# Kernel optimization log

Measured on AMD Instinct MI355X. Metric: run time of the kernel, lower is better.

## Reference

```python
import jax, jax.numpy as jnp
import numpy as np

D_MODEL = 1024
D_FF = 4096


def _layernorm(x, gamma, beta, eps=1e-5):
    mu = jnp.mean(x, axis=-1, keepdims=True)
    var = jnp.var(x, axis=-1, keepdims=True)
    return (x - mu) * jax.lax.rsqrt(var + eps) * gamma + beta


def setup_inputs() -> dict:
    key = jax.random.key(0)
    ks = jax.random.split(key, 7)
    B, S = 4, 2048
    src = jax.random.normal(ks[0], (B, S, D_MODEL), dtype=jnp.float32)
    gamma1 = jnp.ones((D_MODEL,), jnp.float32)
    beta1 = jnp.zeros((D_MODEL,), jnp.float32)
    gamma2 = jnp.ones((D_MODEL,), jnp.float32)
    beta2 = jnp.zeros((D_MODEL,), jnp.float32)
    w1 = jax.random.normal(ks[1], (D_MODEL, D_FF), jnp.float32) * (1.0 / np.sqrt(D_MODEL))
    b1 = jnp.zeros((D_FF,), jnp.float32)
    w2 = jax.random.normal(ks[2], (D_FF, D_MODEL), jnp.float32) * (1.0 / np.sqrt(D_FF))
    b2 = jnp.zeros((D_MODEL,), jnp.float32)
    return {"src": src, "gamma1": gamma1, "beta1": beta1,
            "gamma2": gamma2, "beta2": beta2,
            "w1": w1, "b1": b1, "w2": w2, "b2": b2}


def reference(src, gamma1, beta1, gamma2, beta2, w1, b1, w2, b2):
    # Pre-LN self-attention (single head, Q=K=V=norm_x, no projections)
    norm_x = _layernorm(src, gamma1, beta1)
    dim_k = norm_x.shape[-1]
    scores = jnp.einsum('bqd,bkd->bqk', norm_x, norm_x) / jnp.sqrt(jnp.float32(dim_k))
    weights = jax.nn.softmax(scores, axis=-1)
    attn = jnp.einsum('bqk,bkd->bqd', weights, norm_x)
    x = src + attn  # dropout p=0 -> identity
    # Pre-LN FFN
    h = _layernorm(x, gamma2, beta2)
    h = jax.nn.gelu(h @ w1 + b1, approximate=False)
    h = h @ w2 + b2
    return h + x
```

## Files before the change

kernel.cpp:

```cpp
#include <hip/hip_runtime.h>
#include <hip/hip_bf16.h>
#include <math.h>

typedef __attribute__((ext_vector_type(8))) short s8vec;
typedef __attribute__((ext_vector_type(16))) float f32x16;
typedef __attribute__((ext_vector_type(4))) unsigned short us4;

__device__ __forceinline__ unsigned short f2bf(float f) {
  unsigned u = __float_as_uint(f);
  u = (u + 0x7fffu + ((u >> 16) & 1u)) >> 16;
  return (unsigned short)u;
}
__device__ __forceinline__ float bf2f(unsigned short u) {
  return __uint_as_float(((unsigned)u) << 16);
}

__device__ __forceinline__ float fast_gelu(float t) {
  float t2 = t * t;
  float u = t * (1.59576912f + 0.07135481f * t2);
  float e = __expf(-u);
  return t * __frcp_rn(1.0f + e);
}

__device__ __forceinline__ void async_ld16(const unsigned short* g, unsigned short* l) {
  __builtin_amdgcn_global_load_lds(
      (__attribute__((address_space(1))) void*)g,
      (__attribute__((address_space(3))) void*)l, 16, 0, 0);
}

template <int EPI>
__global__ __launch_bounds__(256) void gemm_nt(
    const unsigned short* __restrict__ A, const unsigned short* __restrict__ B,
    float* __restrict__ outF, unsigned short* __restrict__ outB,
    const float* __restrict__ bias, const float* __restrict__ res,
    int M, int N, int K,
    long long bA, long long bB, long long bO, long long bR, float scale)
{
  __shared__ __align__(16) unsigned short As[128 * 64];
  __shared__ __align__(16) unsigned short Bs[128 * 64];

  const int tid = threadIdx.x;
  const int w = tid >> 6;
  const int l = tid & 63;
  const int z = blockIdx.z;

  A += (size_t)z * bA;
  B += (size_t)z * bB;

  const size_t tileM = (size_t)blockIdx.y * 128;
  const size_t tileN = (size_t)blockIdx.x * 128;

  const int sRow = l >> 3;
  const int sChunk = (l & 7) ^ sRow;
  const unsigned short* aBase = A + (tileM + (w << 5) + sRow) * (size_t)K + (sChunk << 3);
  const unsigned short* bBase = B + (tileN + (w << 5) + sRow) * (size_t)K + (sChunk << 3);
  unsigned short* ldsA = &As[(w << 5) * 64];
  unsigned short* ldsB = &Bs[(w << 5) * 64];

  const int wm = (w >> 1) << 6;
  const int wn = (w & 1) << 6;
  const int fr = l & 31;
  const int fq = l >> 5;

  f32x16 acc[2][2] = {};

  for (int k0 = 0; k0 < K; k0 += 64) {
    __syncthreads();
#pragma unroll
    for (int i = 0; i < 4; ++i) {
      async_ld16(aBase + k0 + (size_t)(i << 3) * K, ldsA + (i << 3) * 64);
      async_ld16(bBase + k0 + (size_t)(i << 3) * K, ldsB + (i << 3) * 64);
    }
    __syncthreads();

#pragma unroll
    for (int s = 0; s < 4; ++s) {
      const int p = ((s << 1) + fq) ^ (fr & 7);
      s8vec af[2], bf[2];
#pragma unroll
      for (int i = 0; i < 2; ++i)
        af[i] = *(const s8vec*)&As[(wm + (i << 5) + fr) * 64 + (p << 3)];
#pragma unroll
      for (int j = 0; j < 2; ++j)
        bf[j] = *(const s8vec*)&Bs[(wn + (j << 5) + fr) * 64 + (p << 3)];
#pragma unroll
      for (int i = 0; i < 2; ++i)
#pragma unroll
        for (int j = 0; j < 2; ++j)
          acc[i][j] = __builtin_amdgcn_mfma_f32_32x32x16_bf16(af[i], bf[j], acc[i][j], 0, 0, 0);
    }
  }

  float* oF = outF + (size_t)z * bO;
  unsigned short* oB = outB + (size_t)z * bO;
  const float* rs = res + (size_t)z * bR;

  float bcol[2];
  if (EPI >= 2) {
#pragma unroll
    for (int j = 0; j < 2; ++j) bcol[j] = bias[tileN + wn + (j << 5) + fr];
  }

#pragma unroll
  for (int i = 0; i < 2; ++i) {
#pragma unroll
    for (int r = 0; r < 16; ++r) {
      const size_t row = tileM + wm + (i << 5) + (r & 3) + ((r >> 2) << 3) + (fq << 2);
      const size_t rb = row * (size_t)N;
#pragma unroll
      for (int j = 0; j < 2; ++j) {
        const size_t col = tileN + wn + (j << 5) + fr;
        const float v = acc[i][j][r];
        if (EPI == 0) {
          oB[rb + col] = f2bf(v * scale);
        } else if (EPI == 1) {
          oF[rb + col] = v + rs[rb + col];
        } else if (EPI == 2) {
          oB[rb + col] = f2bf(fast_gelu(v + bcol[j]));
        } else {
          oF[rb + col] = v + bcol[j] + rs[rb + col];
        }
      }
    }
  }
}

__global__ __launch_bounds__(256) void ln_row(
    const float* __restrict__ x, const float* __restrict__ gamma,
    const float* __restrict__ beta, unsigned short* __restrict__ out)
{
  const int row = blockIdx.x;
  const float4* xr = (const float4*)(x + (size_t)row * 1024);
  const int tid = threadIdx.x;
  float4 v = xr[tid];
  float s = v.x + v.y + v.z + v.w;
  float q = v.x * v.x + v.y * v.y + v.z * v.z + v.w * v.w;
#pragma unroll
  for (int off = 32; off > 0; off >>= 1) {
    s += __shfl_down(s, off);
    q += __shfl_down(q, off);
  }
  __shared__ float rs_[4], rq_[4];
  const int w = tid >> 6, l = tid & 63;
  if (l == 0) { rs_[w] = s; rq_[w] = q; }
  __syncthreads();
  s = rs_[0] + rs_[1] + rs_[2] + rs_[3];
  q = rq_[0] + rq_[1] + rq_[2] + rq_[3];
  const float mu = s * (1.0f / 1024.0f);
  const float var = q * (1.0f / 1024.0f) - mu * mu;
  const float rstd = rsqrtf(var + 1e-5f);
  const float4 g = ((const float4*)gamma)[tid];
  const float4 b = ((const float4*)beta)[tid];
  us4 o;
  o.x = f2bf((v.x - mu) * rstd * g.x + b.x);
  o.y = f2bf((v.y - mu) * rstd * g.y + b.y);
  o.z = f2bf((v.z - mu) * rstd * g.z + b.z);
  o.w = f2bf((v.w - mu) * rstd * g.w + b.w);
  ((us4*)(out + (size_t)row * 1024))[tid] = o;
}

__global__ __launch_bounds__(256) void softmax_row(
    const unsigned short* __restrict__ sc, unsigned short* __restrict__ pr)
{
  const int row = blockIdx.x;
  const s8vec* s8 = (const s8vec*)(sc + (size_t)row * 2048);
  const int tid = threadIdx.x;
  s8vec a = s8[tid];
  float x[8];
#pragma unroll
  for (int i = 0; i < 8; ++i) x[i] = bf2f((unsigned short)a[i]);
  float mx = x[0];
#pragma unroll
  for (int i = 1; i < 8; ++i) mx = fmaxf(mx, x[i]);
#pragma unroll
  for (int off = 32; off > 0; off >>= 1) mx = fmaxf(mx, __shfl_down(mx, off));
  __shared__ float red[4];
  const int w = tid >> 6, l = tid & 63;
  if (l == 0) red[w] = mx;
  __syncthreads();
  mx = fmaxf(fmaxf(red[0], red[1]), fmaxf(red[2], red[3]));
  __syncthreads();
  float e[8], s = 0.f;
#pragma unroll
  for (int i = 0; i < 8; ++i) { e[i] = __expf(x[i] - mx); s += e[i]; }
#pragma unroll
  for (int off = 32; off > 0; off >>= 1) s += __shfl_down(s, off);
  if (l == 0) red[w] = s;
  __syncthreads();
  s = red[0] + red[1] + red[2] + red[3];
  const float inv = 1.0f / s;
  s8vec o;
#pragma unroll
  for (int i = 0; i < 8; ++i) o[i] = (short)f2bf(e[i] * inv);
  ((s8vec*)(pr + (size_t)row * 2048))[tid] = o;
}

template <bool BF16IN>
__global__ __launch_bounds__(256) void transpose_conv(
    const void* __restrict__ in_, unsigned short* __restrict__ out,
    int R, int C, long long bIn, long long bOut)
{
  __shared__ float tile[32][33];
  const int z = blockIdx.z;
  const int tx = threadIdx.x, ty = threadIdx.y;
  const int c0 = blockIdx.x * 32, r0 = blockIdx.y * 32;
  if (BF16IN) {
    const unsigned short* in = (const unsigned short*)in_ + (size_t)z * bIn;
    for (int i = ty; i < 32; i += 8)
      tile[i][tx] = bf2f(in[(size_t)(r0 + i) * C + c0 + tx]);
  } else {
    const float* in = (const float*)in_ + (size_t)z * bIn;
    for (int i = ty; i < 32; i += 8)
      tile[i][tx] = in[(size_t)(r0 + i) * C + c0 + tx];
  }
  __syncthreads();
  unsigned short* o = out + (size_t)z * bOut;
  for (int i = ty; i < 32; i += 8)
    o[(size_t)(c0 + i) * R + r0 + tx] = f2bf(tile[tx][i]);
}

extern "C" void kernel_launch(void* const* d_in, const int* in_sizes, int n_in,
                              void* d_out, int out_size, void* d_ws, size_t ws_size,
                              hipStream_t stream)
{
  (void)in_sizes; (void)n_in; (void)out_size; (void)ws_size;
  const float* src = (const float*)d_in[0];
  const float* g1  = (const float*)d_in[1];
  const float* be1 = (const float*)d_in[2];
  const float* g2  = (const float*)d_in[3];
  const float* be2 = (const float*)d_in[4];
  const float* w1  = (const float*)d_in[5];
  const float* b1  = (const float*)d_in[6];
  const float* w2  = (const float*)d_in[7];
  const float* b2  = (const float*)d_in[8];
  float* out = (float*)d_out;

  char* ws = (char*)d_ws;
  const size_t SZ_NORMX  = (size_t)8192 * 1024 * 2;
  const size_t SZ_SCORES = (size_t)4 * 2048 * 2048 * 4;
  const size_t SZ_PROBS  = (size_t)4 * 2048 * 2048 * 2;
  const size_t SZ_X      = (size_t)8192 * 1024 * 4;
  const size_t SZ_W1T    = (size_t)1024 * 4096 * 2;

  unsigned short* normx  = (unsigned short*)(ws);
  unsigned short* normxT = (unsigned short*)(ws + SZ_NORMX);
  unsigned short* scores = (unsigned short*)(ws + 2 * SZ_NORMX);
  unsigned short* probs  = (unsigned short*)(ws + 2 * SZ_NORMX + SZ_SCORES);
  float*          xbuf   = (float*)(ws + 2 * SZ_NORMX + SZ_SCORES + SZ_PROBS);
  unsigned short* w1t    = (unsigned short*)(ws + 2 * SZ_NORMX + SZ_SCORES + SZ_PROBS + SZ_X);
  unsigned short* w2t    = (unsigned short*)(ws + 2 * SZ_NORMX + SZ_SCORES + SZ_PROBS + SZ_X + SZ_W1T);
  unsigned short* normx2 = normx;
  unsigned short* hbuf   = scores;

  const dim3 tb(32, 8);
  transpose_conv<false><<<dim3(128, 32, 1), tb, 0, stream>>>(w1, w1t, 1024, 4096, 0, 0);
  transpose_conv<false><<<dim3(32, 128, 1), tb, 0, stream>>>(w2, w2t, 4096, 1024, 0, 0);

  ln_row<<<8192, 256, 0, stream>>>(src, g1, be1, normx);
  transpose_conv<true><<<dim3(32, 64, 4), tb, 0, stream>>>(
      normx, normxT, 2048, 1024, (long long)2048 * 1024, (long long)1024 * 2048);

  gemm_nt<0><<<dim3(16, 16, 4), 256, 0, stream>>>(
      normx, normx, nullptr, scores, nullptr, nullptr,
      2048, 2048, 1024,
      (long long)2048 * 1024, (long long)2048 * 1024, (long long)2048 * 2048, 0, 0.03125f);

  softmax_row<<<8192, 256, 0, stream>>>(scores, probs);

  gemm_nt<1><<<dim3(8, 16, 4), 256, 0, stream>>>(
      probs, normxT, xbuf, nullptr, nullptr, src,
      2048, 1024, 2048,
      (long long)2048 * 2048, (long long)1024 * 2048, (long long)2048 * 1024,
      (long long)2048 * 1024, 1.0f);

  ln_row<<<8192, 256, 0, stream>>>(xbuf, g2, be2, normx2);

  gemm_nt<2><<<dim3(32, 64, 1), 256, 0, stream>>>(
      normx2, w1t, nullptr, hbuf, b1, nullptr,
      8192, 4096, 1024, 0, 0, 0, 0, 1.0f);

  gemm_nt<3><<<dim3(8, 64, 1), 256, 0, stream>>>(
      hbuf, w2t, out, nullptr, b2, xbuf,
      8192, 1024, 4096, 0, 0, 0, 0, 1.0f);
}
```

Before: 440.2 us.

## Store GEMM LDS tiles in MFMA fragment order instead of swizzled rows

Reorganizes the shared-memory layout of the A and B tiles so each 32-row by 8-element fragment used by one MFMA is stored contiguously in lane order. Each wave's async global-to-LDS copy now writes exactly the fragment it will read, so reads become simple lane-linear 16-byte loads with no XOR swizzle arithmetic. The intent is to remove bank conflicts and address computation on LDS reads. The trade-off is that each global load now fetches 16 bytes per row at a stride of K across 32 rows, which may reduce coalescing of global memory accesses.

```diff
diff --git a/kernel.cpp b/kernel.cpp
--- a/kernel.cpp
+++ b/kernel.cpp
@@ -36,8 +36,8 @@
     int M, int N, int K,
     long long bA, long long bB, long long bO, long long bR, float scale)
 {
-  __shared__ __align__(16) unsigned short As[128 * 64];
-  __shared__ __align__(16) unsigned short Bs[128 * 64];
+  __shared__ __align__(16) unsigned short As[16 * 512];
+  __shared__ __align__(16) unsigned short Bs[16 * 512];
 
   const int tid = threadIdx.x;
   const int w = tid >> 6;
@@ -50,15 +50,17 @@
   const size_t tileM = (size_t)blockIdx.y * 128;
   const size_t tileN = (size_t)blockIdx.x * 128;
 
-  const int sRow = l >> 3;
-  const int sChunk = (l & 7) ^ sRow;
-  const unsigned short* aBase = A + (tileM + (w << 5) + sRow) * (size_t)K + (sChunk << 3);
-  const unsigned short* bBase = B + (tileN + (w << 5) + sRow) * (size_t)K + (sChunk << 3);
-  unsigned short* ldsA = &As[(w << 5) * 64];
-  unsigned short* ldsB = &Bs[(w << 5) * 64];
-
-  const int wm = (w >> 1) << 6;
-  const int wn = (w & 1) << 6;
+  const int hA = w & 1, iA = w >> 1;
+  const int hB = w >> 1, jB = w & 1;
+  const unsigned short* aSrc = A + (tileM + (hA << 6) + (iA << 5) + (l & 31)) * (size_t)K + ((l >> 5) << 3);
+  const unsigned short* bSrc = B + (tileN + (hB << 6) + (jB << 5) + (l & 31)) * (size_t)K + ((l >> 5) << 3);
+  unsigned short* aDst = &As[(((hA << 1) | iA) << 2) * 512];
+  unsigned short* bDst = &Bs[(((hB << 1) | jB) << 2) * 512];
+
+  const int wmh = w >> 1;
+  const int wnh = w & 1;
+  const unsigned short* aRd = &As[(wmh << 12) + (l << 3)];
+  const unsigned short* bRd = &Bs[(wnh << 12) + (l << 3)];
   const int fr = l & 31;
   const int fq = l >> 5;
 
@@ -67,22 +69,21 @@
   for (int k0 = 0; k0 < K; k0 += 64) {
     __syncthreads();
 #pragma unroll
-    for (int i = 0; i < 4; ++i) {
-      async_ld16(aBase + k0 + (size_t)(i << 3) * K, ldsA + (i << 3) * 64);
-      async_ld16(bBase + k0 + (size_t)(i << 3) * K, ldsB + (i << 3) * 64);
+    for (int s = 0; s < 4; ++s) {
+      async_ld16(aSrc + k0 + (s << 4), aDst + (s << 9));
+      async_ld16(bSrc + k0 + (s << 4), bDst + (s << 9));
     }
     __syncthreads();
 
 #pragma unroll
     for (int s = 0; s < 4; ++s) {
-      const int p = ((s << 1) + fq) ^ (fr & 7);
       s8vec af[2], bf[2];
 #pragma unroll
       for (int i = 0; i < 2; ++i)
-        af[i] = *(const s8vec*)&As[(wm + (i << 5) + fr) * 64 + (p << 3)];
+        af[i] = *(const s8vec*)(aRd + (((i << 2) + s) << 9));
 #pragma unroll
       for (int j = 0; j < 2; ++j)
-        bf[j] = *(const s8vec*)&Bs[(wn + (j << 5) + fr) * 64 + (p << 3)];
+        bf[j] = *(const s8vec*)(bRd + (((j << 2) + s) << 9));
 #pragma unroll
       for (int i = 0; i < 2; ++i)
 #pragma unroll
@@ -94,6 +95,7 @@
   float* oF = outF + (size_t)z * bO;
   unsigned short* oB = outB + (size_t)z * bO;
   const float* rs = res + (size_t)z * bR;
+  const int wm = wmh << 6, wn = wnh << 6;
 
   float bcol[2];
   if (EPI >= 2) {
```

Result: slower. 602.3 us (+36.8%).
